# Kernel optimization log

Hardware: AMD Instinct MI355X
Metric: run time of the kernel (lower is better)

The kernel has to match this reference:

```python
import math
import jax, jax.numpy as jnp
import numpy as np

B, S, H = 8, 2048, 1024
NH = 1
DH = H // NH          # head dim == hidden since NH=1 (required by module's math)
DT = 64               # distance_type


def setup_inputs() -> dict:
    key = jax.random.key(0)
    ks = jax.random.split(key, 10)
    hidden_states = jax.random.normal(ks[0], (B, S, H), dtype=jnp.float32)
    attention_mask = jnp.zeros((B, 1, 1, S), dtype=jnp.float32)
    word_word_relation = jax.random.randint(ks[1], (B, S, S), 0, DT, dtype=jnp.int32)
    init = 0.02
    Wq = jax.random.normal(ks[2], (H, H), dtype=jnp.float32) * init
    bq = jnp.zeros((H,), dtype=jnp.float32)
    Wk = jax.random.normal(ks[3], (H, H), dtype=jnp.float32) * init
    bk = jnp.zeros((H,), dtype=jnp.float32)
    Wv = jax.random.normal(ks[4], (H, H), dtype=jnp.float32) * init
    bv = jnp.zeros((H,), dtype=jnp.float32)
    dist_emb = jax.random.normal(ks[5], (DT, H), dtype=jnp.float32) * init
    dist_emb = dist_emb.at[0].set(0.0)  # padding_idx=0
    return {
        "hidden_states": hidden_states,
        "attention_mask": attention_mask,
        "word_word_relation": word_word_relation,
        "Wq": Wq, "bq": bq, "Wk": Wk, "bk": bk, "Wv": Wv, "bv": bv,
        "dist_emb": dist_emb,
    }


def reference(hidden_states, attention_mask, word_word_relation,
              Wq, bq, Wk, bk, Wv, bv, dist_emb):
    b, s, h = hidden_states.shape
    def heads(x):  # [b,s,h] -> [b,nh,s,dh]
        return x.reshape(b, s, NH, DH).transpose(0, 2, 1, 3)
    q = heads(hidden_states @ Wq.T + bq)
    k = heads(hidden_states @ Wk.T + bk)
    v = heads(hidden_states @ Wv.T + bv)

    scores = jnp.einsum('bhqd,bhkd->bhqk', q, k)                 # [b,nh,s,s]
    word_dot_distance = jnp.einsum('bhqd,td->bhqt', q, dist_emb) # [b,nh,s,DT]

    idx = word_word_relation[:, None, :, :]                      # [b,1,s,s]
    bias = jnp.take_along_axis(word_dot_distance, idx, axis=3)
    mask_out = (word_word_relation == 1)[:, None].astype(scores.dtype)
    bias = bias * mask_out

    scores = (scores + bias) / math.sqrt(DH) + attention_mask
    probs = jax.nn.softmax(scores, axis=-1)
    ctx = jnp.einsum('bhqk,bhkd->bhqd', probs, v)
    ctx = ctx.transpose(0, 2, 1, 3).reshape(b, s, h)
    return ctx
```

## Files before the change

kernel.cpp:

```cpp
#include <hip/hip_runtime.h>

typedef unsigned short u16;
typedef __bf16 bf16x8 __attribute__((ext_vector_type(8)));
typedef u16 u16x8 __attribute__((ext_vector_type(8)));
typedef float f32x4 __attribute__((ext_vector_type(4)));

#define S_LEN 2048
#define H_LEN 1024

__device__ __forceinline__ u16 f2b(float f) {
  unsigned u = __float_as_uint(f);
  return (u16)((u + 0x7FFFu + ((u >> 16) & 1u)) >> 16);
}
__device__ __forceinline__ float b2f(u16 h) { return __uint_as_float(((unsigned)h) << 16); }

#define GLOAD16(gp, lp)                                   \
  __builtin_amdgcn_global_load_lds(                       \
      (__attribute__((address_space(1))) void*)(gp),      \
      (__attribute__((address_space(3))) void*)(lp), 16, 0, 0)

__global__ __launch_bounds__(256) void prep_kernel(
    const float* __restrict__ X, const float* __restrict__ Wq,
    const float* __restrict__ Wk, const float* __restrict__ Wv,
    const float* __restrict__ bq, const float* __restrict__ bk,
    const float* __restrict__ bv, const float* __restrict__ dist,
    const int* __restrict__ rel,
    u16* __restrict__ Xbf, u16* __restrict__ Wbf, float* __restrict__ b_all,
    u16* __restrict__ de1, unsigned* __restrict__ bits, float* __restrict__ d1) {
  size_t tid = (size_t)blockIdx.x * blockDim.x + threadIdx.x;
  size_t nth = (size_t)gridDim.x * blockDim.x;
  for (size_t i = tid; i < 4194304u; i += nth) {
    float4 v = ((const float4*)X)[i];
    ushort4 o; o.x = f2b(v.x); o.y = f2b(v.y); o.z = f2b(v.z); o.w = f2b(v.w);
    ((ushort4*)Xbf)[i] = o;
  }
  for (size_t i = tid; i < 786432u; i += nth) {
    int which = (int)(i >> 18);
    size_t off = i & 262143u;
    const float4* src = (const float4*)(which == 0 ? Wq : (which == 1 ? Wk : Wv));
    float4 v = src[off];
    ushort4 o; o.x = f2b(v.x); o.y = f2b(v.y); o.z = f2b(v.z); o.w = f2b(v.w);
    ((ushort4*)Wbf)[i] = o;
  }
  const int4* r4 = (const int4*)rel;
  for (size_t wi = tid; wi < 1048576u; wi += nth) {
    const int4* s = r4 + wi * 8;
    unsigned m = 0;
#pragma unroll
    for (int u = 0; u < 8; ++u) {
      int4 v = s[u];
      m |= (unsigned)(v.x == 1) << (u * 4 + 0);
      m |= (unsigned)(v.y == 1) << (u * 4 + 1);
      m |= (unsigned)(v.z == 1) << (u * 4 + 2);
      m |= (unsigned)(v.w == 1) << (u * 4 + 3);
    }
    bits[wi] = m;
  }
  for (size_t i = tid; i < 256u; i += nth) {
    float4 v = ((const float4*)(dist + H_LEN))[i];
    ushort4 o; o.x = f2b(v.x); o.y = f2b(v.y); o.z = f2b(v.z); o.w = f2b(v.w);
    ((ushort4*)de1)[i] = o;
  }
  for (size_t i = tid; i < 3072u; i += nth)
    b_all[i] = (i < 1024) ? bq[i] : (i < 2048 ? bk[i - 1024] : bv[i - 2048]);
  for (size_t i = tid; i < 16384u; i += nth) d1[i] = 0.f;
}

struct GArgs {
  const u16* A; const u16* B;
  long long sA, sB;
  int ldA, ldB, K;
  u16 *Qo, *Ko, *Vo; const float* b_all; const u16* de1; float* d1;
  const unsigned* relbits; const float* mask; u16* P;
  float* outp;
};

template <int EPI>
__global__ __launch_bounds__(256) void gemm_nt(GArgs g) {
  const int bz = blockIdx.z;
  int bx = blockIdx.x, by = blockIdx.y;
  if constexpr (EPI == 0) {
    const int lin = by * 24 + bx;
    const int band = lin / (24 * 8), rem = lin % (24 * 8);
    by = band * 8 + (rem & 7);
    bx = rem >> 3;
  }
  const u16* Abase = g.A + (size_t)bz * g.sA;
  const u16* Bbase = g.B + (size_t)bz * g.sB;
  const int m0 = by * 128, n0 = bx * 128;

  __shared__ u16 smem[16384];
  u16* As = smem;
  u16* Bs = smem + 8192;

  const int tid = threadIdx.x;
  const int lane = tid & 63, w = tid >> 6;
  const int wm = w >> 1, wn = w & 1;
  const int l15 = lane & 15, quad = lane >> 4;

  f32x4 acc[4][4];
  f32x4 acc_sum[4];
  const f32x4 zero = {0.f, 0.f, 0.f, 0.f};
#pragma unroll
  for (int a = 0; a < 4; ++a) {
    acc_sum[a] = zero;
#pragma unroll
    for (int b = 0; b < 4; ++b) acc[a][b] = zero;
  }
  bf16x8 ones;
#pragma unroll
  for (int i = 0; i < 8; ++i) ones[i] = (__bf16)1.0f;

  const int c0 = tid, c1 = tid + 256;
  const u16* ga0 = Abase + (size_t)(m0 + (c0 >> 2)) * g.ldA + (c0 & 3) * 8;
  const u16* ga1 = Abase + (size_t)(m0 + (c1 >> 2)) * g.ldA + (c1 & 3) * 8;
  const u16* gb0 = Bbase + (size_t)(n0 + (c0 >> 2)) * g.ldB + (c0 & 3) * 8;
  const u16* gb1 = Bbase + (size_t)(n0 + (c1 >> 2)) * g.ldB + (c1 & 3) * 8;
  u16* la0 = As + c0 * 8; u16* la1 = As + c1 * 8;
  u16* lb0 = Bs + c0 * 8; u16* lb1 = Bs + c1 * 8;

  for (int kt = 0; kt < g.K; kt += 64) {
    __syncthreads();
    GLOAD16(ga0 + kt, la0);      GLOAD16(ga0 + kt + 32, la0 + 4096);
    GLOAD16(ga1 + kt, la1);      GLOAD16(ga1 + kt + 32, la1 + 4096);
    GLOAD16(gb0 + kt, lb0);      GLOAD16(gb0 + kt + 32, lb0 + 4096);
    GLOAD16(gb1 + kt, lb1);      GLOAD16(gb1 + kt + 32, lb1 + 4096);
    __syncthreads();
#pragma unroll
    for (int s = 0; s < 2; ++s) {
      bf16x8 af[4], bfb[4];
#pragma unroll
      for (int t = 0; t < 4; ++t) {
        af[t]  = *(const bf16x8*)&As[s * 4096 + (wm * 64 + t * 16 + l15) * 32 + quad * 8];
        bfb[t] = *(const bf16x8*)&Bs[s * 4096 + (wn * 64 + t * 16 + l15) * 32 + quad * 8];
      }
#pragma unroll
      for (int mt = 0; mt < 4; ++mt) {
#pragma unroll
        for (int nt = 0; nt < 4; ++nt)
          acc[mt][nt] = __builtin_amdgcn_mfma_f32_16x16x32_bf16(af[mt], bfb[nt], acc[mt][nt], 0, 0, 0);
        if constexpr (EPI == 2)
          acc_sum[mt] = __builtin_amdgcn_mfma_f32_16x16x32_bf16(af[mt], ones, acc_sum[mt], 0, 0, 0);
      }
    }
  }
  __syncthreads();

  const int nbase = n0 + wn * 64;

  if constexpr (EPI == 0) {
    const int which = n0 >> 10;
    float bv4[4], dw[4];
#pragma unroll
    for (int nt = 0; nt < 4; ++nt) {
      bv4[nt] = g.b_all[nbase + nt * 16 + l15];
      dw[nt] = (which == 0) ? b2f(g.de1[nbase + nt * 16 + l15]) : 0.f;
    }
#pragma unroll
    for (int mt = 0; mt < 4; ++mt)
#pragma unroll
      for (int r = 0; r < 4; ++r) {
        const int row = wm * 64 + mt * 16 + quad * 4 + r;
        float part = 0.f;
#pragma unroll
        for (int nt = 0; nt < 4; ++nt) {
          const float v = acc[mt][nt][r] + bv4[nt];
          part += v * dw[nt];
          const int col = wn * 64 + nt * 16 + l15;
          const int chunkS = (col >> 3) ^ (row & 15);
          smem[row * 128 + chunkS * 8 + (col & 7)] = f2b(v);
        }
        if (which == 0) {
          part += __shfl_xor(part, 1);
          part += __shfl_xor(part, 2);
          part += __shfl_xor(part, 4);
          part += __shfl_xor(part, 8);
          if (l15 == 0) atomicAdd(&g.d1[m0 + row], part);
        }
      }
    __syncthreads();
    u16* dstbuf = which == 0 ? g.Qo : (which == 1 ? g.Ko : g.Vo);
    const int nl0 = n0 & 1023;
#pragma unroll
    for (int p = 0; p < 8; ++p) {
      const int flat = p * 256 + tid;
      const int row = flat >> 4, chunk = flat & 15;
      const int chunkS = chunk ^ (row & 15);
      u16x8 v = *(const u16x8*)&smem[row * 128 + chunkS * 8];
      *(u16x8*)(dstbuf + (size_t)(m0 + row) * H_LEN + nl0 + chunk * 8) = v;
    }
  }

  if constexpr (EPI == 1) {
    float mk[4];
#pragma unroll
    for (int nt = 0; nt < 4; ++nt) mk[nt] = g.mask[bz * S_LEN + nbase + nt * 16 + l15];
    const size_t bSS = (size_t)bz * S_LEN * S_LEN;
#pragma unroll
    for (int mt = 0; mt < 4; ++mt)
#pragma unroll
      for (int r = 0; r < 4; ++r) {
        const int row = wm * 64 + mt * 16 + quad * 4 + r;
        const int gi = bz * S_LEN + m0 + row;
        const float d1v = g.d1[gi] * 0.03125f;
        const unsigned w0 = g.relbits[(size_t)gi * 64 + (nbase >> 5)];
        const unsigned w1 = g.relbits[(size_t)gi * 64 + (nbase >> 5) + 1];
#pragma unroll
        for (int nt = 0; nt < 4; ++nt) {
          const unsigned word = (nt & 2) ? w1 : w0;
          const int pos = (nt * 16 + l15) & 31;
          const float bias = ((word >> pos) & 1) ? d1v : 0.f;
          const float logit = acc[mt][nt][r] * 0.03125f + bias + mk[nt];
          const float pv = __expf(logit);
          const int col = wn * 64 + nt * 16 + l15;
          const int chunkS = (col >> 3) ^ (row & 15);
          smem[row * 128 + chunkS * 8 + (col & 7)] = f2b(pv);
        }
      }
    __syncthreads();
#pragma unroll
    for (int p = 0; p < 8; ++p) {
      const int flat = p * 256 + tid;
      const int row = flat >> 4, chunk = flat & 15;
      const int chunkS = chunk ^ (row & 15);
      u16x8 v = *(const u16x8*)&smem[row * 128 + chunkS * 8];
      *(u16x8*)(g.P + bSS + (size_t)(m0 + row) * S_LEN + n0 + chunk * 8) = v;
    }
  }

  if constexpr (EPI == 2) {
    const size_t ob = (size_t)bz * S_LEN * H_LEN;
#pragma unroll
    for (int mt = 0; mt < 4; ++mt)
#pragma unroll
      for (int r = 0; r < 4; ++r) {
        const int i = m0 + wm * 64 + mt * 16 + quad * 4 + r;
        const float inv = 1.0f / acc_sum[mt][r];
        const size_t rowo = ob + (size_t)i * H_LEN;
#pragma unroll
        for (int nt = 0; nt < 4; ++nt) {
          const int d = n0 + wn * 64 + nt * 16 + l15;
          g.outp[rowo + d] = acc[mt][nt][r] * inv;
        }
      }
  }
}

__global__ __launch_bounds__(256) void transpose_v(const u16* __restrict__ V,
                                                   u16* __restrict__ Vt) {
  const int b = blockIdx.z;
  const int j0 = blockIdx.x * 64;
  const int d0 = blockIdx.y * 64;
  __shared__ u16 t[64][72];
  const int tid = threadIdx.x;
  const int tr = tid >> 4;
  const int tc = (tid & 15) * 4;
#pragma unroll
  for (int p = 0; p < 4; ++p) {
    const int jl = p * 16 + tr;
    const u16* src = V + ((size_t)b * S_LEN + (j0 + jl)) * H_LEN + d0 + tc;
    ushort4 v = *(const ushort4*)src;
    t[jl][tc + 0] = v.x; t[jl][tc + 1] = v.y; t[jl][tc + 2] = v.z; t[jl][tc + 3] = v.w;
  }
  __syncthreads();
#pragma unroll
  for (int p = 0; p < 4; ++p) {
    const int dl = p * 16 + tr;
    ushort4 v;
    v.x = t[tc + 0][dl]; v.y = t[tc + 1][dl]; v.z = t[tc + 2][dl]; v.w = t[tc + 3][dl];
    *(ushort4*)(Vt + ((size_t)b * H_LEN + (d0 + dl)) * S_LEN + j0 + tc) = v;
  }
}

extern "C" void kernel_launch(void* const* d_in, const int* in_sizes, int n_in,
                              void* d_out, int out_size, void* d_ws, size_t ws_size,
                              hipStream_t stream) {
  (void)in_sizes; (void)n_in; (void)out_size; (void)ws_size;
  const float* X    = (const float*)d_in[0];
  const float* mask = (const float*)d_in[1];
  const int*   rel  = (const int*)d_in[2];
  const float* Wq   = (const float*)d_in[3];
  const float* bq   = (const float*)d_in[4];
  const float* Wk   = (const float*)d_in[5];
  const float* bk   = (const float*)d_in[6];
  const float* Wv   = (const float*)d_in[7];
  const float* bv   = (const float*)d_in[8];
  const float* dist = (const float*)d_in[9];
  float* out = (float*)d_out;

  char* p = (char*)d_ws;
  u16* Xbf = (u16*)p;      p += (size_t)16384 * 1024 * 2;
  u16* Wbf = (u16*)p;      p += (size_t)3072 * 1024 * 2;
  float* b_all = (float*)p; p += 3072 * 4;
  u16* de1 = (u16*)p;      p += 4096;
  u16* Qb = (u16*)p;       p += (size_t)16384 * 1024 * 2;
  u16* Kb = (u16*)p;       p += (size_t)16384 * 1024 * 2;
  u16* Vb = (u16*)p;       p += (size_t)16384 * 1024 * 2;
  u16* Vt = (u16*)p;       p += (size_t)16384 * 1024 * 2;
  float* d1 = (float*)p;   p += 16384 * 4;
  unsigned* relbits = (unsigned*)p; p += (size_t)1048576 * 4;
  u16* P = (u16*)p;        p += (size_t)8 * 2048 * 2048 * 2;

  prep_kernel<<<1024, 256, 0, stream>>>(X, Wq, Wk, Wv, bq, bk, bv, dist, rel,
                                        Xbf, Wbf, b_all, de1, relbits, d1);

  GArgs g0 = {};
  g0.A = Xbf; g0.B = Wbf; g0.sA = 0; g0.sB = 0;
  g0.ldA = 1024; g0.ldB = 1024; g0.K = 1024;
  g0.Qo = Qb; g0.Ko = Kb; g0.Vo = Vb; g0.b_all = b_all; g0.de1 = de1; g0.d1 = d1;
  gemm_nt<0><<<dim3(24, 128, 1), dim3(256, 1, 1), 0, stream>>>(g0);

  transpose_v<<<dim3(32, 16, 8), dim3(256, 1, 1), 0, stream>>>(Vb, Vt);

  GArgs g1 = {};
  g1.A = Qb; g1.B = Kb; g1.sA = 2048LL * 1024; g1.sB = 2048LL * 1024;
  g1.ldA = 1024; g1.ldB = 1024; g1.K = 1024;
  g1.relbits = relbits; g1.d1 = d1; g1.mask = mask; g1.P = P;
  gemm_nt<1><<<dim3(16, 16, 8), dim3(256, 1, 1), 0, stream>>>(g1);

  GArgs g2 = {};
  g2.A = P; g2.B = Vt; g2.sA = 2048LL * 2048; g2.sB = 1024LL * 2048;
  g2.ldA = 2048; g2.ldB = 2048; g2.K = 2048;
  g2.outp = out;
  gemm_nt<2><<<dim3(8, 16, 8), dim3(256, 1, 1), 0, stream>>>(g2);
}
```

Baseline: 631.1 us.

## Fuse V transpose into projection epilogue and precompute softmax row sums

The QKV projection epilogue now writes V directly in transposed layout, which removes the separate transpose kernel and the intermediate V buffer. The QK^T epilogue reduces per-row partial sums of the exponentials into a psums buffer. The PV GEMM reads those sums instead of running an extra MFMA against a ones vector per tile. Block indices are remapped so batch is the fastest-varying dimension, and the LDS swizzle is changed to reduce bank conflicts, including on the new transposed read path. The cost is strided 2-byte LDS gathers in the V epilogue and an extra psums buffer round trip through global memory.

Result: slower. 663.5 us (+5.1%).

```diff
diff --git a/kernel.cpp b/kernel.cpp
--- a/kernel.cpp
+++ b/kernel.cpp
@@ -13,6 +13,10 @@
   return (u16)((u + 0x7FFFu + ((u >> 16) & 1u)) >> 16);
 }
 __device__ __forceinline__ float b2f(u16 h) { return __uint_as_float(((unsigned)h) << 16); }
+
+__device__ __forceinline__ int csw(int colgrp, int row) {
+  return colgrp ^ (((row >> 3) + (row & 7)) & 15);
+}
 
 #define GLOAD16(gp, lp)                                   \
   __builtin_amdgcn_global_load_lds(                       \
@@ -69,21 +73,27 @@
 struct GArgs {
   const u16* A; const u16* B;
   long long sA, sB;
-  int ldA, ldB, K;
-  u16 *Qo, *Ko, *Vo; const float* b_all; const u16* de1; float* d1;
-  const unsigned* relbits; const float* mask; u16* P;
+  int ldA, ldB, K, nbits;
+  u16 *Qo, *Ko, *Vt; const float* b_all; const u16* de1; float* d1;
+  const unsigned* relbits; const float* mask; u16* P; float* psums;
   float* outp;
 };
 
 template <int EPI>
 __global__ __launch_bounds__(256) void gemm_nt(GArgs g) {
-  const int bz = blockIdx.z;
-  int bx = blockIdx.x, by = blockIdx.y;
+  int bx, by, bz;
   if constexpr (EPI == 0) {
-    const int lin = by * 24 + bx;
+    bz = 0;
+    const int lin = blockIdx.y * 24 + blockIdx.x;
     const int band = lin / (24 * 8), rem = lin % (24 * 8);
     by = band * 8 + (rem & 7);
     bx = rem >> 3;
+  } else {
+    const int lin = blockIdx.x;
+    bz = lin & 7;
+    const int loc = lin >> 3;
+    bx = loc & ((1 << g.nbits) - 1);
+    by = loc >> g.nbits;
   }
   const u16* Abase = g.A + (size_t)bz * g.sA;
   const u16* Bbase = g.B + (size_t)bz * g.sB;
@@ -99,17 +109,11 @@
   const int l15 = lane & 15, quad = lane >> 4;
 
   f32x4 acc[4][4];
-  f32x4 acc_sum[4];
   const f32x4 zero = {0.f, 0.f, 0.f, 0.f};
 #pragma unroll
-  for (int a = 0; a < 4; ++a) {
-    acc_sum[a] = zero;
+  for (int a = 0; a < 4; ++a)
 #pragma unroll
     for (int b = 0; b < 4; ++b) acc[a][b] = zero;
-  }
-  bf16x8 ones;
-#pragma unroll
-  for (int i = 0; i < 8; ++i) ones[i] = (__bf16)1.0f;
 
   const int c0 = tid, c1 = tid + 256;
   const u16* ga0 = Abase + (size_t)(m0 + (c0 >> 2)) * g.ldA + (c0 & 3) * 8;
@@ -135,13 +139,10 @@
         bfb[t] = *(const bf16x8*)&Bs[s * 4096 + (wn * 64 + t * 16 + l15) * 32 + quad * 8];
       }
 #pragma unroll
-      for (int mt = 0; mt < 4; ++mt) {
+      for (int mt = 0; mt < 4; ++mt)
 #pragma unroll
         for (int nt = 0; nt < 4; ++nt)
           acc[mt][nt] = __builtin_amdgcn_mfma_f32_16x16x32_bf16(af[mt], bfb[nt], acc[mt][nt], 0, 0, 0);
-        if constexpr (EPI == 2)
-          acc_sum[mt] = __builtin_amdgcn_mfma_f32_16x16x32_bf16(af[mt], ones, acc_sum[mt], 0, 0, 0);
-      }
     }
   }
   __syncthreads();
@@ -167,8 +168,7 @@
           const float v = acc[mt][nt][r] + bv4[nt];
           part += v * dw[nt];
           const int col = wn * 64 + nt * 16 + l15;
-          const int chunkS = (col >> 3) ^ (row & 15);
-          smem[row * 128 + chunkS * 8 + (col & 7)] = f2b(v);
+          smem[row * 128 + csw(col >> 3, row) * 8 + (col & 7)] = f2b(v);
         }
         if (which == 0) {
           part += __shfl_xor(part, 1);
@@ -179,15 +179,30 @@
         }
       }
     __syncthreads();
-    u16* dstbuf = which == 0 ? g.Qo : (which == 1 ? g.Ko : g.Vo);
-    const int nl0 = n0 & 1023;
-#pragma unroll
-    for (int p = 0; p < 8; ++p) {
-      const int flat = p * 256 + tid;
-      const int row = flat >> 4, chunk = flat & 15;
-      const int chunkS = chunk ^ (row & 15);
-      u16x8 v = *(const u16x8*)&smem[row * 128 + chunkS * 8];
-      *(u16x8*)(dstbuf + (size_t)(m0 + row) * H_LEN + nl0 + chunk * 8) = v;
+    if (which < 2) {
+      u16* dstbuf = which == 0 ? g.Qo : g.Ko;
+      const int nl0 = n0 & 1023;
+#pragma unroll
+      for (int p = 0; p < 8; ++p) {
+        const int flat = p * 256 + tid;
+        const int row = flat >> 4, chunk = flat & 15;
+        u16x8 v = *(const u16x8*)&smem[row * 128 + csw(chunk, row) * 8];
+        *(u16x8*)(dstbuf + (size_t)(m0 + row) * H_LEN + nl0 + chunk * 8) = v;
+      }
+    } else {
+      const int b = m0 >> 11, j0 = m0 & 2047, dg0 = n0 - 2048;
+#pragma unroll
+      for (int p = 0; p < 8; ++p) {
+        const int flat = p * 256 + tid;
+        const int dcol = flat >> 4, ich = flat & 15;
+        u16x8 v;
+#pragma unroll
+        for (int s = 0; s < 8; ++s) {
+          const int row = ich * 8 + s;
+          v[s] = smem[row * 128 + csw(dcol >> 3, row) * 8 + (dcol & 7)];
+        }
+        *(u16x8*)(g.Vt + ((size_t)b * H_LEN + dg0 + dcol) * S_LEN + j0 + ich * 8) = v;
+      }
     }
   }
 
@@ -205,6 +220,7 @@
         const float d1v = g.d1[gi] * 0.03125f;
         const unsigned w0 = g.relbits[(size_t)gi * 64 + (nbase >> 5)];
         const unsigned w1 = g.relbits[(size_t)gi * 64 + (nbase >> 5) + 1];
+        float psum = 0.f;
 #pragma unroll
         for (int nt = 0; nt < 4; ++nt) {
           const unsigned word = (nt & 2) ? w1 : w0;
@@ -212,18 +228,22 @@
           const float bias = ((word >> pos) & 1) ? d1v : 0.f;
           const float logit = acc[mt][nt][r] * 0.03125f + bias + mk[nt];
           const float pv = __expf(logit);
+          psum += pv;
           const int col = wn * 64 + nt * 16 + l15;
-          const int chunkS = (col >> 3) ^ (row & 15);
-          smem[row * 128 + chunkS * 8 + (col & 7)] = f2b(pv);
-        }
+          smem[row * 128 + csw(col >> 3, row) * 8 + (col & 7)] = f2b(pv);
+        }
+        psum += __shfl_xor(psum, 1);
+        psum += __shfl_xor(psum, 2);
+        psum += __shfl_xor(psum, 4);
+        psum += __shfl_xor(psum, 8);
+        if (l15 == 0) g.psums[(size_t)gi * 32 + bx * 2 + wn] = psum;
       }
     __syncthreads();
 #pragma unroll
     for (int p = 0; p < 8; ++p) {
       const int flat = p * 256 + tid;
       const int row = flat >> 4, chunk = flat & 15;
-      const int chunkS = chunk ^ (row & 15);
-      u16x8 v = *(const u16x8*)&smem[row * 128 + chunkS * 8];
+      u16x8 v = *(const u16x8*)&smem[row * 128 + csw(chunk, row) * 8];
       *(u16x8*)(g.P + bSS + (size_t)(m0 + row) * S_LEN + n0 + chunk * 8) = v;
     }
   }
@@ -235,7 +255,13 @@
 #pragma unroll
       for (int r = 0; r < 4; ++r) {
         const int i = m0 + wm * 64 + mt * 16 + quad * 4 + r;
-        const float inv = 1.0f / acc_sum[mt][r];
+        const size_t gi = (size_t)bz * S_LEN + i;
+        float part = g.psums[gi * 32 + l15] + g.psums[gi * 32 + 16 + l15];
+        part += __shfl_xor(part, 1);
+        part += __shfl_xor(part, 2);
+        part += __shfl_xor(part, 4);
+        part += __shfl_xor(part, 8);
+        const float inv = 1.0f / part;
         const size_t rowo = ob + (size_t)i * H_LEN;
 #pragma unroll
         for (int nt = 0; nt < 4; ++nt) {
@@ -243,32 +269,6 @@
           g.outp[rowo + d] = acc[mt][nt][r] * inv;
         }
       }
-  }
-}
-
-__global__ __launch_bounds__(256) void transpose_v(const u16* __restrict__ V,
-                                                   u16* __restrict__ Vt) {
-  const int b = blockIdx.z;
-  const int j0 = blockIdx.x * 64;
-  const int d0 = blockIdx.y * 64;
-  __shared__ u16 t[64][72];
-  const int tid = threadIdx.x;
-  const int tr = tid >> 4;
-  const int tc = (tid & 15) * 4;
-#pragma unroll
-  for (int p = 0; p < 4; ++p) {
-    const int jl = p * 16 + tr;
-    const u16* src = V + ((size_t)b * S_LEN + (j0 + jl)) * H_LEN + d0 + tc;
-    ushort4 v = *(const ushort4*)src;
-    t[jl][tc + 0] = v.x; t[jl][tc + 1] = v.y; t[jl][tc + 2] = v.z; t[jl][tc + 3] = v.w;
-  }
-  __syncthreads();
-#pragma unroll
-  for (int p = 0; p < 4; ++p) {
-    const int dl = p * 16 + tr;
-    ushort4 v;
-    v.x = t[tc + 0][dl]; v.y = t[tc + 1][dl]; v.z = t[tc + 2][dl]; v.w = t[tc + 3][dl];
-    *(ushort4*)(Vt + ((size_t)b * H_LEN + (d0 + dl)) * S_LEN + j0 + tc) = v;
   }
 }
 
@@ -295,9 +295,9 @@
   u16* de1 = (u16*)p;      p += 4096;
   u16* Qb = (u16*)p;       p += (size_t)16384 * 1024 * 2;
   u16* Kb = (u16*)p;       p += (size_t)16384 * 1024 * 2;
-  u16* Vb = (u16*)p;       p += (size_t)16384 * 1024 * 2;
   u16* Vt = (u16*)p;       p += (size_t)16384 * 1024 * 2;
   float* d1 = (float*)p;   p += 16384 * 4;
+  float* psums = (float*)p; p += (size_t)16384 * 32 * 4;
   unsigned* relbits = (unsigned*)p; p += (size_t)1048576 * 4;
   u16* P = (u16*)p;        p += (size_t)8 * 2048 * 2048 * 2;
 
@@ -307,20 +307,18 @@
   GArgs g0 = {};
   g0.A = Xbf; g0.B = Wbf; g0.sA = 0; g0.sB = 0;
   g0.ldA = 1024; g0.ldB = 1024; g0.K = 1024;
-  g0.Qo = Qb; g0.Ko = Kb; g0.Vo = Vb; g0.b_all = b_all; g0.de1 = de1; g0.d1 = d1;
+  g0.Qo = Qb; g0.Ko = Kb; g0.Vt = Vt; g0.b_all = b_all; g0.de1 = de1; g0.d1 = d1;
   gemm_nt<0><<<dim3(24, 128, 1), dim3(256, 1, 1), 0, stream>>>(g0);
-
-  transpose_v<<<dim3(32, 16, 8), dim3(256, 1, 1), 0, stream>>>(Vb, Vt);
 
   GArgs g1 = {};
   g1.A = Qb; g1.B = Kb; g1.sA = 2048LL * 1024; g1.sB = 2048LL * 1024;
-  g1.ldA = 1024; g1.ldB = 1024; g1.K = 1024;
-  g1.relbits = relbits; g1.d1 = d1; g1.mask = mask; g1.P = P;
-  gemm_nt<1><<<dim3(16, 16, 8), dim3(256, 1, 1), 0, stream>>>(g1);
+  g1.ldA = 1024; g1.ldB = 1024; g1.K = 1024; g1.nbits = 4;
+  g1.relbits = relbits; g1.d1 = d1; g1.mask = mask; g1.P = P; g1.psums = psums;
+  gemm_nt<1><<<dim3(2048, 1, 1), dim3(256, 1, 1), 0, stream>>>(g1);
 
   GArgs g2 = {};
   g2.A = P; g2.B = Vt; g2.sA = 2048LL * 2048; g2.sB = 1024LL * 2048;
-  g2.ldA = 2048; g2.ldB = 2048; g2.K = 2048;
-  g2.outp = out;
-  gemm_nt<2><<<dim3(8, 16, 8), dim3(256, 1, 1), 0, stream>>>(g2);
-}
+  g2.ldA = 2048; g2.ldB = 2048; g2.K = 2048; g2.nbits = 3;
+  g2.psums = psums; g2.outp = out;
+  gemm_nt<2><<<dim3(1024, 1, 1), dim3(256, 1, 1), 0, stream>>>(g2);
+}
```
